# Optimization experiments

Measured on AMD Instinct MI355X. Metric: run time of the kernel, lower is better.

## Reference

```python
import jax, jax.numpy as jnp
import numpy as np

SR = 16000
N_FFT = 1024
HOP = 256
WIN = 1024
N_MELS = 80
EPS = 1e-8
DRY_W, RIR_W = 3.0, 1.0
TIME_W, FREQ_W, MEL_W = 1.0, 0.5, 0.3
CONSIST_W, RIR_REG_W = 0.2, 0.1


def _hann(n):
    # torch.hann_window(periodic=True)
    return (0.5 - 0.5 * jnp.cos(2.0 * jnp.pi * jnp.arange(n) / n)).astype(jnp.float32)


def _stft(x):
    """torchaudio.transforms.Spectrogram(power=None, normalized=True) equivalent.
    x: [..., T] -> complex [..., n_freqs, n_frames]"""
    shp = x.shape
    T = shp[-1]
    xf = x.reshape(-1, T)
    pad = N_FFT // 2
    xp = jnp.pad(xf, ((0, 0), (pad, pad)), mode='reflect')  # center=True
    n_frames = 1 + T // HOP
    idx = jnp.arange(n_frames)[:, None] * HOP + jnp.arange(N_FFT)[None, :]
    win = _hann(WIN)
    frames = xp[:, idx] * win[None, None, :]              # [N, frames, n_fft]
    spec = jnp.fft.rfft(frames, axis=-1)                  # [N, frames, freqs]
    spec = spec / jnp.sqrt(jnp.sum(win ** 2))             # normalized='window'
    return spec.reshape(shp[:-1] + (n_frames, N_FFT // 2 + 1)).swapaxes(-1, -2)


def _mel_fb():
    # torchaudio melscale_fbanks, htk scale, norm=None, f_min=0, f_max=sr/2
    n_freqs = N_FFT // 2 + 1
    all_freqs = np.linspace(0.0, SR / 2.0, n_freqs)
    hz2mel = lambda f: 2595.0 * np.log10(1.0 + f / 700.0)
    mel2hz = lambda m: 700.0 * (10.0 ** (m / 2595.0) - 1.0)
    m_pts = np.linspace(hz2mel(0.0), hz2mel(SR / 2.0), N_MELS + 2)
    f_pts = mel2hz(m_pts)
    f_diff = f_pts[1:] - f_pts[:-1]
    slopes = f_pts[None, :] - all_freqs[:, None]
    down = -slopes[:, :-2] / f_diff[:-1]
    up = slopes[:, 2:] / f_diff[1:]
    fb = np.maximum(0.0, np.minimum(down, up))
    return jnp.asarray(fb, jnp.float32)  # [n_freqs, n_mels]

_FB = _mel_fb()


def _l1(a, b):
    return jnp.mean(jnp.abs(a - b))


def _freq_loss(pred, target):
    ps, ts = _stft(pred), _stft(target)
    mag_loss = _l1(jnp.abs(ps), jnp.abs(ts))
    dphi = jnp.angle(ps) - jnp.angle(ts)
    # cosine sim of unit [cos, sin] vectors == cos(delta phase)
    phase_loss = 1.0 - jnp.mean(jnp.cos(dphi))
    return mag_loss + 0.1 * phase_loss


def _mel_loss(pred, target):
    pm = jnp.einsum('...ft,fm->...mt', jnp.abs(_stft(pred)) ** 2, _FB)
    tm = jnp.einsum('...ft,fm->...mt', jnp.abs(_stft(target)) ** 2, _FB)
    return _l1(jnp.log(pm + EPS), jnp.log(tm + EPS))


def _consistency_loss(pred_dry, pred_rir, mix):
    # full linear convolution along time, truncated to first T samples
    T = pred_dry.shape[-1]
    n = 2 * T
    D = jnp.fft.rfft(pred_dry, n=n, axis=-1)
    R = jnp.fft.rfft(pred_rir, n=n, axis=-1)
    rec = jnp.fft.irfft(D * R, n=n, axis=-1)[..., :T]
    return _l1(rec, mix[..., :T])


def _rir_reg_loss(pred_rir):
    T = pred_rir.shape[-1]
    sparsity = jnp.mean(jnp.abs(pred_rir))
    seg = T // 4
    decay = 0.0
    for i in range(3):
        e1 = jnp.mean(pred_rir[:, :, i * seg:(i + 1) * seg] ** 2)
        e2 = jnp.mean(pred_rir[:, :, (i + 1) * seg:(i + 2) * seg] ** 2)
        decay = decay + jax.nn.relu(e2 - 0.8 * e1)
    return sparsity + decay


def setup_inputs() -> dict:
    key = jax.random.key(0)
    ks = jax.random.split(key, 5)
    shape = (32, 2, 64000)
    names = ['pred_dry', 'pred_rir', 'target_dry', 'target_rir', 'mix']
    return {n: jax.random.normal(k, shape, dtype=jnp.float32) for n, k in zip(names, ks)}


def reference(pred_dry, pred_rir, target_dry, target_rir, mix):
    dry_time = _l1(pred_dry, target_dry)
    dry_freq = _freq_loss(pred_dry, target_dry)
    dry_mel = _mel_loss(pred_dry, target_dry)
    total_dry = TIME_W * dry_time + FREQ_W * dry_freq + MEL_W * dry_mel

    rir_time = _l1(pred_rir, target_rir)
    rir_reg = _rir_reg_loss(pred_rir)
    total_rir = rir_time + RIR_REG_W * rir_reg

    consist = _consistency_loss(pred_dry, pred_rir, mix)
    total = DRY_W * total_dry + RIR_W * total_rir + CONSIST_W * consist
    return total
```

## Files before the change

### kernel.cpp

```cpp
#include <hip/hip_runtime.h>
#include <math.h>

#define ROWS 64
#define TLEN 64000
#define NFR 251
#define NMELS 80
#define NFB 131072
#define PI2F 6.28318530717958647692f
#define PI_F 3.14159265358979323846f

__device__ double g_part[64][12];

__device__ constexpr int DR[16] = {0,4,8,12,1,5,9,13,2,6,10,14,3,7,11,15};
__device__ constexpr int RM[16] = {0,3,2,1,15,14,13,12,11,10,9,8,7,6,5,4};

__device__ inline int dr4(int i){ return ((i & 3) << 2) | (i >> 2); }
__device__ inline int SW(int k){ return k + (k >> 5); }

__device__ inline void atomAddD(double* p, double v){
  __hip_atomic_fetch_add(p, v, __ATOMIC_RELAXED, __HIP_MEMORY_SCOPE_AGENT);
}
__device__ inline int brev6(int x){ return (int)((unsigned)__brev((unsigned)x) >> 26); }
__device__ inline float2 cmul(float2 a, float2 b){
  return make_float2(a.x*b.x - a.y*b.y, a.x*b.y + a.y*b.x);
}
__device__ inline float wred(float v){
#pragma unroll
  for (int o = 32; o > 0; o >>= 1) v += __shfl_down(v, o, 64);
  return v;
}

__device__ inline void wave_fence(){
  asm volatile("s_waitcnt lgkmcnt(0)" ::: "memory");
  __builtin_amdgcn_sched_barrier(0);
}

template<int S, int N>
__device__ inline void fft64_lanes(float2* v, int l){
  float2 W[5];
#pragma unroll
  for (int si = 0; si < 5; ++si){
    int d = 32 >> si;
    float a = (float)S * PI_F * (float)(l & (d-1)) * (1.0f/(float)d);
    float sn, cs; __sincosf(a, &sn, &cs);
    W[si] = make_float2(cs, sn);
  }
#pragma unroll
  for (int si = 0; si < 6; ++si){
    int d = 32 >> si;
    bool hi = (l & d) != 0;
#pragma unroll
    for (int rr = 0; rr < N; ++rr){
      float2 x = v[rr];
      float tx = __shfl_xor(x.x, d, 64);
      float ty = __shfl_xor(x.y, d, 64);
      float sx = x.x + tx, sy = x.y + ty;
      float dx = tx - x.x, dy = ty - x.y;
      float rx, ry;
      if (si < 5){ rx = dx*W[si].x - dy*W[si].y; ry = dx*W[si].y + dy*W[si].x; }
      else       { rx = dx; ry = dy; }
      v[rr].x = hi ? rx : sx;
      v[rr].y = hi ? ry : sy;
    }
  }
}

template<int S>
__device__ inline void fft16_reg(float2* v){
  const float Sf = (float)S;
  const float C1 = 0.9238795325112867f, S1 = 0.3826834323650898f, C2 = 0.7071067811865476f;
  const float2 W1[4] = {{1.f,0.f},{C1,Sf*S1},{C2,Sf*C2},{S1,Sf*C1}};
  const float2 W2[4] = {{1.f,0.f},{C2,Sf*C2},{0.f,Sf},{-C2,Sf*C2}};
  const float2 W3[4] = {{1.f,0.f},{S1,Sf*C1},{-C2,Sf*C2},{-C1,-Sf*S1}};
#pragma unroll
  for (int j = 0; j < 4; ++j){
    float2 x0=v[j], x1=v[j+4], x2=v[j+8], x3=v[j+12];
    float2 t0={x0.x+x2.x, x0.y+x2.y}, t1={x0.x-x2.x, x0.y-x2.y};
    float2 t2={x1.x+x3.x, x1.y+x3.y}, t3={x1.x-x3.x, x1.y-x3.y};
    float2 y0={t0.x+t2.x, t0.y+t2.y};
    float2 y2={t0.x-t2.x, t0.y-t2.y};
    float2 y1={t1.x - Sf*t3.y, t1.y + Sf*t3.x};
    float2 y3={t1.x + Sf*t3.y, t1.y - Sf*t3.x};
    v[j]=y0; v[j+4]=cmul(y1,W1[j]); v[j+8]=cmul(y2,W2[j]); v[j+12]=cmul(y3,W3[j]);
  }
#pragma unroll
  for (int b = 0; b < 4; ++b){
    float2 x0=v[4*b], x1=v[4*b+1], x2=v[4*b+2], x3=v[4*b+3];
    float2 t0={x0.x+x2.x, x0.y+x2.y}, t1={x0.x-x2.x, x0.y-x2.y};
    float2 t2={x1.x+x3.x, x1.y+x3.y}, t3={x1.x-x3.x, x1.y-x3.y};
    v[4*b]   = make_float2(t0.x+t2.x, t0.y+t2.y);
    v[4*b+2] = make_float2(t0.x-t2.x, t0.y-t2.y);
    v[4*b+1] = make_float2(t1.x - Sf*t3.y, t1.y + Sf*t3.x);
    v[4*b+3] = make_float2(t1.x + Sf*t3.y, t1.y - Sf*t3.x);
  }
}

template<int S>
__device__ inline void fft128_wave(float2* v, int l){
  float2 a = {v[0].x+v[1].x, v[0].y+v[1].y};
  float2 b = {v[0].x-v[1].x, v[0].y-v[1].y};
  float ang = (float)S * PI_F * (float)l * (1.0f/64.0f);
  float sn, cs; __sincosf(ang, &sn, &cs);
  v[0] = a; v[1] = cmul(b, make_float2(cs, sn));
  fft64_lanes<S,2>(v, l);
}

template<int S>
__device__ inline void fft8p(float2* y){
  const float Sf = (float)S;
  const float C2 = 0.7071067811865476f;
  float2 t0={y[0].x+y[4].x, y[0].y+y[4].y};
  float2 t1={y[1].x+y[5].x, y[1].y+y[5].y};
  float2 t2={y[2].x+y[6].x, y[2].y+y[6].y};
  float2 t3={y[3].x+y[7].x, y[3].y+y[7].y};
  float2 u0={y[0].x-y[4].x, y[0].y-y[4].y};
  float2 u1={y[1].x-y[5].x, y[1].y-y[5].y};
  float2 u2={y[2].x-y[6].x, y[2].y-y[6].y};
  float2 u3={y[3].x-y[7].x, y[3].y-y[7].y};
  { float x=u1.x, yy=u1.y; u1.x = C2*(x - Sf*yy); u1.y = C2*(Sf*x + yy); }
  { float x=u2.x, yy=u2.y; u2.x = -Sf*yy;         u2.y = Sf*x; }
  { float x=u3.x, yy=u3.y; u3.x = -C2*(x + Sf*yy); u3.y = C2*(Sf*x - yy); }
  {
    float2 e0={t0.x+t2.x,t0.y+t2.y}, e1={t0.x-t2.x,t0.y-t2.y};
    float2 o0={t1.x+t3.x,t1.y+t3.y}, o1={t1.x-t3.x,t1.y-t3.y};
    y[0]=make_float2(e0.x+o0.x, e0.y+o0.y);
    y[4]=make_float2(e0.x-o0.x, e0.y-o0.y);
    y[2]=make_float2(e1.x - Sf*o1.y, e1.y + Sf*o1.x);
    y[6]=make_float2(e1.x + Sf*o1.y, e1.y - Sf*o1.x);
  }
  {
    float2 e0={u0.x+u2.x,u0.y+u2.y}, e1={u0.x-u2.x,u0.y-u2.y};
    float2 o0={u1.x+u3.x,u1.y+u3.y}, o1={u1.x-u3.x,u1.y-u3.y};
    y[1]=make_float2(e0.x+o0.x, e0.y+o0.y);
    y[5]=make_float2(e0.x-o0.x, e0.y-o0.y);
    y[3]=make_float2(e1.x - Sf*o1.y, e1.y + Sf*o1.x);
    y[7]=make_float2(e1.x + Sf*o1.y, e1.y - Sf*o1.x);
  }
}

template<int S>
__device__ inline void fft64_lds(float2* v, int l, float2* scr){
  int s = l >> 3, a = l & 7;
  int sw = (s & 1);
#pragma unroll
  for (int h = 0; h < 2; ++h){
    float2* vh = v + 8*h;
#pragma unroll
    for (int r = 0; r < 8; ++r) scr[r*64 + l] = vh[r];
    wave_fence();
    float2 y[8];
#pragma unroll
    for (int j = 0; j < 8; ++j)
      y[j] = scr[s*64 + a + 8*((j + s) & 7)];
    fft8p<S>(y);
    {
      float ang = (float)S * PI2F * (float)l * (1.0f/64.0f);
      float sn, cs; __sincosf(ang, &sn, &cs);
      float2 b1 = make_float2(cs, sn), cur = b1;
#pragma unroll
      for (int c = 1; c < 8; ++c){
        y[c] = cmul(y[c], cur);
        if (c < 7) cur = cmul(cur, b1);
      }
    }
    wave_fence();
#pragma unroll
    for (int c = 0; c < 8; ++c)
      scr[s*64 + a + 8*(c ^ sw)] = y[c];
    wave_fence();
    float2 z[8];
#pragma unroll
    for (int j = 0; j < 8; ++j)
      z[j] = scr[s*64 + ((j + s) & 7) + 8*(a ^ sw)];
    fft8p<S>(z);
    {
      float ang2 = (float)S * PI2F * (float)s * 0.125f;
      float sn2, cs2; __sincosf(ang2, &sn2, &cs2);
      float2 b2 = make_float2(cs2, sn2), cur = b2;
#pragma unroll
      for (int d = 1; d < 8; ++d){
        z[d] = cmul(z[d], cur);
        if (d < 7) cur = cmul(cur, b2);
      }
    }
    wave_fence();
#pragma unroll
    for (int d = 0; d < 8; ++d)
      scr[s*64 + a + 8*(d ^ sw)] = z[d];
    wave_fence();
#pragma unroll
    for (int r = 0; r < 8; ++r)
      vh[r] = scr[r*64 + (l ^ ((r & 1) << 3))];
    wave_fence();
  }
}

template<int S>
__device__ inline void fft1024_lds(float2* v, int l, float2* scr){
  fft16_reg<S>(v);
  float a = (float)S * PI2F * (float)l * (1.0f/1024.0f);
  float sn, cs; __sincosf(a, &sn, &cs);
  float2 T = make_float2(cs, sn);
  float2 cur = T;
#pragma unroll
  for (int k2 = 1; k2 < 16; ++k2){
    v[DR[k2]] = cmul(v[DR[k2]], cur);
    if (k2 < 15) cur = cmul(cur, T);
  }
  fft64_lds<S>(v, l, scr);
}

__device__ inline void r4p(float2* v, int i0, int i1, int i2, int i3){
  float2 x0=v[i0], x1=v[i1], x2=v[i2], x3=v[i3];
  float2 t0={x0.x+x2.x, x0.y+x2.y}, t1={x0.x-x2.x, x0.y-x2.y};
  float2 t2={x1.x+x3.x, x1.y+x3.y}, t3={x1.x-x3.x, x1.y-x3.y};
  v[i0] = make_float2(t0.x+t2.x, t0.y+t2.y);
  v[i2] = make_float2(t0.x-t2.x, t0.y-t2.y);
  v[i1] = make_float2(t1.x - t3.y, t1.y + t3.x);
  v[i3] = make_float2(t1.x + t3.y, t1.y - t3.x);
}

__device__ inline void ifft16_reg(float2* v){
#pragma unroll
  for (int b = 0; b < 4; ++b) r4p(v, 4*b, 4*b+1, 4*b+2, 4*b+3);
  const float C1 = 0.9238795325112867f, S1 = 0.3826834323650898f, C2 = 0.7071067811865476f;
  const float2 W1[4] = {{1.f,0.f},{C1,S1},{C2,C2},{S1,C1}};
  const float2 W2[4] = {{1.f,0.f},{C2,C2},{0.f,1.f},{-C2,C2}};
  const float2 W3[4] = {{1.f,0.f},{S1,C1},{-C2,C2},{-C1,-S1}};
#pragma unroll
  for (int j = 1; j < 4; ++j){
    v[j+4]  = cmul(v[j+4],  W1[j]);
    v[j+8]  = cmul(v[j+8],  W2[j]);
    v[j+12] = cmul(v[j+12], W3[j]);
  }
#pragma unroll
  for (int j = 0; j < 4; ++j) r4p(v, j, j+4, j+8, j+12);
}

__device__ inline void ifft1024_lds(float2* v, int l, float2* scr){
  fft64_lds<1>(v, l, scr);
  float a = PI2F * (float)l * (1.0f/1024.0f);
  float sn, cs; __sincosf(a, &sn, &cs);
  float2 T = make_float2(cs, sn);
  float2 cur = T;
#pragma unroll
  for (int k2 = 1; k2 < 16; ++k2){
    v[DR[k2]] = cmul(v[DR[k2]], cur);
    if (k2 < 15) cur = cmul(cur, T);
  }
  ifft16_reg(v);
}

template<int N>
__device__ inline void ifft64_lanes(float2* v, int l){
  float2 W[5];
#pragma unroll
  for (int si = 0; si < 5; ++si){
    int d = 32 >> si;
    float a = PI_F * (float)(l & (d-1)) * (1.0f/(float)d);
    float sn, cs; __sincosf(a, &sn, &cs);
    W[si] = make_float2(cs, sn);
  }
#pragma unroll
  for (int si = 5; si >= 0; --si){
    int d = 32 >> si;
    bool hi = (l & d) != 0;
#pragma unroll
    for (int rr = 0; rr < N; ++rr){
      float2 x = v[rr];
      float2 xp = x;
      if (si < 5 && hi) xp = cmul(x, W[si]);
      float tx = __shfl_xor(xp.x, d, 64);
      float ty = __shfl_xor(xp.y, d, 64);
      v[rr].x = hi ? (tx - xp.x) : (xp.x + tx);
      v[rr].y = hi ? (ty - xp.y) : (xp.y + ty);
    }
  }
}

__device__ inline void ifft128_wave(float2* v, int l){
  ifft64_lanes<2>(v, l);
  float ang = PI_F * (float)l * (1.0f/64.0f);
  float sn, cs; __sincosf(ang, &sn, &cs);
  v[1] = cmul(v[1], make_float2(cs, sn));
  float2 a = {v[0].x+v[1].x, v[0].y+v[1].y};
  float2 b = {v[0].x-v[1].x, v[0].y-v[1].y};
  v[0] = a; v[1] = b;
}

extern "C" __global__ void __launch_bounds__(256) k_init(){
  int t = blockIdx.x*256 + threadIdx.x;
  if (t < 768) ((double*)g_part)[t] = 0.0;
}

extern "C" __global__ void __launch_bounds__(256) k_time(
    const float* __restrict__ pd, const float* __restrict__ td,
    const float* __restrict__ pr, const float* __restrict__ tr){
  const int N4 = ROWS*TLEN/4;
  int stride = gridDim.x * 256;
  float sdt=0.f, srt=0.f, ssp=0.f, e0=0.f, e1=0.f, e2=0.f, e3=0.f;
  const float4* pd4 = (const float4*)pd;
  const float4* td4 = (const float4*)td;
  const float4* pr4 = (const float4*)pr;
  const float4* tr4 = (const float4*)tr;
  for (int i = blockIdx.x*256 + threadIdx.x; i < N4; i += stride){
    float4 a = pd4[i], b = td4[i], p = pr4[i], q = tr4[i];
    sdt += fabsf(a.x-b.x)+fabsf(a.y-b.y)+fabsf(a.z-b.z)+fabsf(a.w-b.w);
    srt += fabsf(p.x-q.x)+fabsf(p.y-q.y)+fabsf(p.z-q.z)+fabsf(p.w-q.w);
    ssp += fabsf(p.x)+fabsf(p.y)+fabsf(p.z)+fabsf(p.w);
    float p2 = p.x*p.x + p.y*p.y + p.z*p.z + p.w*p.w;
    int seg = (i % 16000) / 4000;
    if (seg == 0) e0 += p2; else if (seg == 1) e1 += p2;
    else if (seg == 2) e2 += p2; else e3 += p2;
  }
  sdt = wred(sdt); srt = wred(srt); ssp = wred(ssp);
  e0 = wred(e0); e1 = wred(e1); e2 = wred(e2); e3 = wred(e3);
  if ((threadIdx.x & 63) == 0){
    int bank = (blockIdx.x*4 + (threadIdx.x >> 6)) & 63;
    atomAddD(&g_part[bank][0], (double)sdt);
    atomAddD(&g_part[bank][1], (double)srt);
    atomAddD(&g_part[bank][2], (double)ssp);
    atomAddD(&g_part[bank][3], (double)e0);
    atomAddD(&g_part[bank][4], (double)e1);
    atomAddD(&g_part[bank][5], (double)e2);
    atomAddD(&g_part[bank][6], (double)e3);
  }
}

extern "C" __global__ void __launch_bounds__(64) k_stft(
    const float* __restrict__ pd, const float* __restrict__ td){
  __shared__ float2 scr[512];
  __shared__ float2 spec0[64];
  __shared__ float2 pt[530];
  int l = threadIdx.x;
  int frame = (blockIdx.x & 7) * (ROWS*NFR/8) + (blockIdx.x >> 3);
  int r = frame / NFR, fr = frame - r*NFR;
  const float* pdr = pd + (size_t)r*TLEN;
  const float* tdr = td + (size_t)r*TLEN;
  const float scale = 0.05103103630798288f;
  int base = fr*256 - 512;
  float2 v[16];
#pragma unroll
  for (int m = 0; m < 16; ++m){
    int j = l + 64*m;
    int g = base + j;
    g = (g < 0) ? -g : ((g >= TLEN) ? (2*TLEN - 2 - g) : g);
    float w = (0.5f - 0.5f*__cosf((PI2F/1024.0f)*(float)j)) * scale;
    v[m] = make_float2(pdr[g]*w, tdr[g]*w);
  }
  fft1024_lds<-1>(v, l, scr);
  spec0[l] = v[0];
  float magp = 0.f, cosp = 0.f;
#pragma unroll
  for (int rr = 1; rr < 16; ++rr){
    float2 z = v[rr];
    float2 zm;
    zm.x = __shfl_xor(v[RM[rr]].x, 63, 64);
    zm.y = __shfl_xor(v[RM[rr]].y, 63, 64);
    int k = DR[rr] + 16*l;
    float px = 0.5f*(z.x + zm.x), py = 0.5f*(z.y - zm.y);
    float tx = 0.5f*(z.y + zm.y), ty = -0.5f*(z.x - zm.x);
    float ppk = px*px + py*py, ttk = tx*tx + ty*ty;
    float rp = rsqrtf(fmaxf(ppk, 1e-30f)), rt = rsqrtf(fmaxf(ttk, 1e-30f));
    magp += 0.5f*fabsf(ppk*rp - ttk*rt);
    cosp += 0.5f*((px*tx + py*ty)*rp*rt);
    int kk = (k <= 512) ? k : 1024 - k;
    pt[SW(kk)] = make_float2(ppk, ttk);
  }
  if (l <= 32){
    float2 z  = spec0[l];
    float2 zm = spec0[(64 - l) & 63];
    float px = 0.5f*(z.x + zm.x), py = 0.5f*(z.y - zm.y);
    float tx = 0.5f*(z.y + zm.y), ty = -0.5f*(z.x - zm.x);
    float ppk = px*px + py*py, ttk = tx*tx + ty*ty;
    float rp = rsqrtf(fmaxf(ppk, 1e-30f)), rt = rsqrtf(fmaxf(ttk, 1e-30f));
    magp += fabsf(ppk*rp - ttk*rt);
    cosp += (px*tx + py*ty)*rp*rt;
    pt[SW(16*l)] = make_float2(ppk, ttk);
  }
  float melp = 0.f;
  const float C = (2595.0f * log10f(1.0f + 8000.0f/700.0f))
                  * (1.0f/81.0f) * (1.0f/2595.0f) * 2.302585093f;
  const float df = 15.625f;
  {
    int m = l;
    float f0 = 700.0f*(__expf(C*(float)(m  )) - 1.0f);
    float f1 = 700.0f*(__expf(C*(float)(m+1)) - 1.0f);
    float f2 = 700.0f*(__expf(C*(float)(m+2)) - 1.0f);
    float i1 = 1.0f/(f1 - f0), i2 = 1.0f/(f2 - f1);
    int lo = (int)ceilf(f0 * (1.0f/df));  if (lo < 0) lo = 0;
    int hi = (int)floorf(f2 * (1.0f/df)); if (hi > 512) hi = 512;
    float pm = 0.f, tm = 0.f;
#pragma unroll 2
    for (int k = lo; k <= hi; ++k){
      float frq = df*(float)k;
      float c = fmaxf(fminf((frq - f0)*i1, (f2 - frq)*i2), 0.f);
      float2 w = pt[SW(k)];
      pm += c*w.x; tm += c*w.y;
    }
    melp += fabsf(__logf(pm + 1e-8f) - __logf(tm + 1e-8f));
  }
  {
    int m = 64 + (l >> 2), q = l & 3;
    float f0 = 700.0f*(__expf(C*(float)(m  )) - 1.0f);
    float f1 = 700.0f*(__expf(C*(float)(m+1)) - 1.0f);
    float f2 = 700.0f*(__expf(C*(float)(m+2)) - 1.0f);
    float i1 = 1.0f/(f1 - f0), i2 = 1.0f/(f2 - f1);
    int lo = (int)ceilf(f0 * (1.0f/df));  if (lo < 0) lo = 0;
    int hi = (int)floorf(f2 * (1.0f/df)); if (hi > 512) hi = 512;
    int n = hi - lo + 1;
    int ch = (n + 3) >> 2;
    int k0 = lo + q*ch;
    int k1 = k0 + ch; if (k1 > hi + 1) k1 = hi + 1;
    float pm = 0.f, tm = 0.f;
#pragma unroll 2
    for (int k = k0; k < k1; ++k){
      float frq = df*(float)k;
      float c = fmaxf(fminf((frq - f0)*i1, (f2 - frq)*i2), 0.f);
      float2 w = pt[SW(k)];
      pm += c*w.x; tm += c*w.y;
    }
    pm += __shfl_xor(pm, 1, 64); pm += __shfl_xor(pm, 2, 64);
    tm += __shfl_xor(tm, 1, 64); tm += __shfl_xor(tm, 2, 64);
    if (q == 0)
      melp += fabsf(__logf(pm + 1e-8f) - __logf(tm + 1e-8f));
  }
  magp = wred(magp); cosp = wred(cosp); melp = wred(melp);
  if (l == 0){
    int bank = blockIdx.x & 63;
    atomAddD(&g_part[bank][7], (double)magp);
    atomAddD(&g_part[bank][8], (double)cosp);
    atomAddD(&g_part[bank][9], (double)melp);
  }
}

extern "C" __global__ void __launch_bounds__(512) k_fwd1(
    const float* __restrict__ pd, const float* __restrict__ pr,
    float2* __restrict__ buf, int row0){
  __shared__ float SM[10256];
  float* LA = SM;
  float* LB = SM + 5000;
  float2* LT = (float2*)SM;
  int wid = threadIdx.x >> 6, l = threadIdx.x & 63;
  int tid = threadIdx.x;
  float2* scr = (float2*)SM + (size_t)wid*512;
  int rl = blockIdx.y;
  int n1base = blockIdx.x * 8;
  int n1 = n1base + wid;
  const float* a = pd + (size_t)(row0+rl)*TLEN;
  const float* b = pr + (size_t)(row0+rl)*TLEN;
  for (int i = tid; i < 2000; i += 512){
    int n2 = i >> 2, wp = (i & 3)*2;
    float2 va = *(const float2*)&a[n1base + wp + 128*n2];
    float2 vb = *(const float2*)&b[n1base + wp + 128*n2];
    *(float2*)&LA[n2*10 + wp] = va;
    *(float2*)&LB[n2*10 + wp] = vb;
  }
  __syncthreads();
  float2 v[16];
#pragma unroll
  for (int m = 0; m < 16; ++m){
    int n2 = l + 64*m;
    if (n2 < 500) v[m] = make_float2(LA[n2*10 + wid], LB[n2*10 + wid]);
    else          v[m] = make_float2(0.f, 0.f);
  }
  __syncthreads();
  fft1024_lds<-1>(v, l, scr);
  const float tw = -(PI2F / (float)NFB);
#pragma unroll
  for (int rr = 0; rr < 16; ++rr){
    int K = DR[rr] + 16*l;
    float ang = tw * (float)(n1*K);
    float sn, cs; __sincosf(ang, &sn, &cs);
    v[rr] = cmul(v[rr], make_float2(cs, sn));
  }
  float2* rowp = buf + (size_t)rl*NFB;
  __syncthreads();
#pragma unroll
  for (int c = 0; c < 2; ++c){
#pragma unroll
    for (int rrl = 0; rrl < 8; ++rrl)
      LT[wid*513 + rrl*64 + l] = v[c*8 + rrl];
    __syncthreads();
#pragma unroll
    for (int it = 0; it < 4; ++it){
      int g = (tid + it*512)*2;
      int s = g >> 3, nw = g & 7;
      float2 x = LT[nw*513 + s], y = LT[(nw+1)*513 + s];
      *(float4*)&rowp[(size_t)(c*512 + s)*128 + n1base + nw] =
          make_float4(x.x, x.y, y.x, y.y);
    }
    __syncthreads();
  }
}

__device__ inline float2 pointmul(float2 z, float2 zm){
  float Dx = 0.5f*(z.x + zm.x), Dy = 0.5f*(z.y - zm.y);
  float Rx = 0.5f*(z.y + zm.y), Ry = -0.5f*(z.x - zm.x);
  return make_float2(Dx*Rx - Dy*Ry, Dx*Ry + Dy*Rx);
}

extern "C" __global__ void __launch_bounds__(256) k_mid(float2* __restrict__ buf){
  int wid = threadIdx.x >> 6, l = threadIdx.x & 63;
  int p = blockIdx.x*4 + wid;
  if (p > 512) return;
  int k2A = p, k2B = (1024 - p) & 1023;
  int sA = dr4(k2A & 15)*64 + (k2A >> 4);
  int sB = dr4(k2B & 15)*64 + (k2B >> 4);
  float2* base = buf + (size_t)blockIdx.y*NFB;
  float2* rA = base + (size_t)sA*128;
  float2* rB = base + (size_t)sB*128;
  bool pair = (sB != sA);
  float2 vA[2] = { rA[l], rA[l+64] };
  float2 vB[2];
  if (pair){ vB[0] = rB[l]; vB[1] = rB[l+64]; }
  fft128_wave<-1>(vA, l);
  if (pair) fft128_wave<-1>(vB, l);
  float2 cA[2];
  if (p == 0){
    int kb = brev6(l);
    int q0 = brev6((64 - kb) & 63);
    float2 zm0 = { __shfl(vA[0].x, q0, 64), __shfl(vA[0].y, q0, 64) };
    float2 zm1 = { __shfl_xor(vA[1].x, 63, 64), __shfl_xor(vA[1].y, 63, 64) };
    cA[0] = pointmul(vA[0], zm0);
    cA[1] = pointmul(vA[1], zm1);
  } else {
    const float2* src = pair ? vB : vA;
    float2 zm0 = { __shfl_xor(src[1].x, 63, 64), __shfl_xor(src[1].y, 63, 64) };
    float2 zm1 = { __shfl_xor(src[0].x, 63, 64), __shfl_xor(src[0].y, 63, 64) };
    cA[0] = pointmul(vA[0], zm0);
    cA[1] = pointmul(vA[1], zm1);
  }
  float2 cB[2];
  if (pair){
    cB[0] = make_float2( __shfl_xor(cA[1].x, 63, 64), -__shfl_xor(cA[1].y, 63, 64) );
    cB[1] = make_float2( __shfl_xor(cA[0].x, 63, 64), -__shfl_xor(cA[0].y, 63, 64) );
  }
  const float twi = PI2F / (float)NFB;
  ifft128_wave(cA, l);
#pragma unroll
  for (int rr = 0; rr < 2; ++rr){
    int n1 = l + 64*rr;
    float ang = twi * (float)(n1*k2A);
    float sn, cs; __sincosf(ang, &sn, &cs);
    rA[n1] = cmul(cA[rr], make_float2(cs, sn));
  }
  if (pair){
    ifft128_wave(cB, l);
#pragma unroll
    for (int rr = 0; rr < 2; ++rr){
      int n1 = l + 64*rr;
      float ang = twi * (float)(n1*k2B);
      float sn, cs; __sincosf(ang, &sn, &cs);
      rB[n1] = cmul(cB[rr], make_float2(cs, sn));
    }
  }
}

extern "C" __global__ void __launch_bounds__(512) k_inv2(
    const float* __restrict__ mix, float2* __restrict__ buf, int row0){
  __shared__ float SM[13208];
  float2* LT = (float2*)SM;
  float* LM = SM + 8208;
  int wid = threadIdx.x >> 6, l = threadIdx.x & 63;
  int tid = threadIdx.x;
  float2* scr = (float2*)SM + (size_t)wid*512;
  int rl = blockIdx.y;
  int n1base = blockIdx.x * 8;
  float2* rowp = buf + (size_t)rl*NFB;
  float2 v[16];
#pragma unroll
  for (int c = 0; c < 2; ++c){
#pragma unroll
    for (int it = 0; it < 4; ++it){
      int g = (tid + it*512)*2;
      int s = g >> 3, nw = g & 7;
      float4 q = *(const float4*)&rowp[(size_t)(c*512 + s)*128 + n1base + nw];
      LT[nw*513 + s]     = make_float2(q.x, q.y);
      LT[(nw+1)*513 + s] = make_float2(q.z, q.w);
    }
    __syncthreads();
#pragma unroll
    for (int rrl = 0; rrl < 8; ++rrl)
      v[c*8 + rrl] = LT[wid*513 + rrl*64 + l];
    __syncthreads();
  }
  const float* mr = mix + (size_t)(row0+rl)*TLEN;
  for (int i = tid; i < 2000; i += 512){
    int n2 = i >> 2, wp = (i & 3)*2;
    *(float2*)&LM[n2*10 + wp] = *(const float2*)&mr[n1base + wp + 128*n2];
  }
  ifft1024_lds(v, l, scr);
  __syncthreads();
  const float invn = 1.0f/(float)NFB;
  float acc = 0.f;
#pragma unroll
  for (int m = 0; m < 16; ++m){
    int n2 = l + 64*m;
    if (n2 < 500)
      acc += fabsf(v[m].x*invn - LM[n2*10 + wid]);
  }
  acc = wred(acc);
  if (l == 0){
    int bank = (blockIdx.x*8 + wid + blockIdx.y*16) & 63;
    atomAddD(&g_part[bank][10], (double)acc);
  }
}

extern "C" __global__ void __launch_bounds__(64) k_finalize(float* __restrict__ out){
  __shared__ double s[12];
  int t = threadIdx.x;
  if (t < 12){
    double v = 0.0;
    for (int b = 0; b < 64; ++b) v += g_part[b][t];
    s[t] = v;
  }
  __syncthreads();
  if (t == 0){
    double dt = s[0] / 4096000.0;
    double rt = s[1] / 4096000.0;
    double sp = s[2] / 4096000.0;
    double e0 = s[3] / 1024000.0, e1 = s[4] / 1024000.0;
    double e2 = s[5] / 1024000.0, e3 = s[6] / 1024000.0;
    double dec = fmax(e1 - 0.8*e0, 0.0) + fmax(e2 - 0.8*e1, 0.0) + fmax(e3 - 0.8*e2, 0.0);
    double c1 = 8240832.0;
    double freq = s[7]/c1 + 0.1*(1.0 - s[8]/c1);
    double mel  = s[9] / 1285120.0;
    double cons = s[10] / 4096000.0;
    double total = 3.0*(dt + 0.5*freq + 0.3*mel)
                 + (rt + 0.1*(sp + dec))
                 + 0.2*cons;
    out[0] = (float)total;
  }
}

extern "C" void kernel_launch(void* const* d_in, const int* in_sizes, int n_in,
                              void* d_out, int out_size, void* d_ws, size_t ws_size,
                              hipStream_t stream){
  const float* pd = (const float*)d_in[0];
  const float* pr = (const float*)d_in[1];
  const float* td = (const float*)d_in[2];
  const float* tr = (const float*)d_in[3];
  const float* mx = (const float*)d_in[4];
  float* out = (float*)d_out;
  float2* buf = (float2*)d_ws;

  size_t rowBytes = (size_t)NFB * sizeof(float2);
  int maxrows = (int)(ws_size / rowBytes);
  if (maxrows > ROWS) maxrows = ROWS;
  if (maxrows < 1) maxrows = 1;
  int nch = (ROWS + maxrows - 1) / maxrows;
  int chrows = (ROWS + nch - 1) / nch;

  hipLaunchKernelGGL(k_init, dim3(3), dim3(256), 0, stream);
  hipLaunchKernelGGL(k_time, dim3(2048), dim3(256), 0, stream, pd, td, pr, tr);
  hipLaunchKernelGGL(k_stft, dim3(ROWS*NFR), dim3(64), 0, stream, pd, td);
  for (int row0 = 0; row0 < ROWS; row0 += chrows){
    int nr = ROWS - row0; if (nr > chrows) nr = chrows;
    hipLaunchKernelGGL(k_fwd1, dim3(16, nr),  dim3(512), 0, stream, pd, pr, buf, row0);
    hipLaunchKernelGGL(k_mid,  dim3(129, nr), dim3(256), 0, stream, buf);
    hipLaunchKernelGGL(k_inv2, dim3(16, nr),  dim3(512), 0, stream, mx, buf, row0);
  }
  hipLaunchKernelGGL(k_finalize, dim3(1), dim3(64), 0, stream, out);
}
```

Measured before the change: 285.8 us.

## Pack two real inverse FFT columns into one complex IFFT in consistency loss

The inverse stage exploits the conjugate symmetry of real outputs. k_mid no longer runs a second 128-point IFFT for the paired column and instead writes the conjugate of the first. k_inv2 combines two adjacent columns as a + i*b into one complex sequence, runs half as many 1024-point IFFTs with 256 threads, and reads the real and imaginary parts as the two real time signals. It also drops a sched_barrier in wave_fence and picks power-of-two chunk row counts. This halves FFT work and LDS use in the inverse path, at the risk of subtle indexing or sign errors in the packing.

Measured after the change: 273.3 us. 1.05x faster.

```diff
diff --git a/kernel.cpp b/kernel.cpp
--- a/kernel.cpp
+++ b/kernel.cpp
@@ -32,7 +32,6 @@
 
 __device__ inline void wave_fence(){
   asm volatile("s_waitcnt lgkmcnt(0)" ::: "memory");
-  __builtin_amdgcn_sched_barrier(0);
 }
 
 template<int S, int N>
@@ -531,11 +530,6 @@
     cA[0] = pointmul(vA[0], zm0);
     cA[1] = pointmul(vA[1], zm1);
   }
-  float2 cB[2];
-  if (pair){
-    cB[0] = make_float2( __shfl_xor(cA[1].x, 63, 64), -__shfl_xor(cA[1].y, 63, 64) );
-    cB[1] = make_float2( __shfl_xor(cA[0].x, 63, 64), -__shfl_xor(cA[0].y, 63, 64) );
-  }
   const float twi = PI2F / (float)NFB;
   ifft128_wave(cA, l);
 #pragma unroll
@@ -543,25 +537,17 @@
     int n1 = l + 64*rr;
     float ang = twi * (float)(n1*k2A);
     float sn, cs; __sincosf(ang, &sn, &cs);
-    rA[n1] = cmul(cA[rr], make_float2(cs, sn));
-  }
-  if (pair){
-    ifft128_wave(cB, l);
-#pragma unroll
-    for (int rr = 0; rr < 2; ++rr){
-      int n1 = l + 64*rr;
-      float ang = twi * (float)(n1*k2B);
-      float sn, cs; __sincosf(ang, &sn, &cs);
-      rB[n1] = cmul(cB[rr], make_float2(cs, sn));
-    }
-  }
-}
-
-extern "C" __global__ void __launch_bounds__(512) k_inv2(
+    float2 val = cmul(cA[rr], make_float2(cs, sn));
+    rA[n1] = val;
+    if (pair) rB[n1] = make_float2(val.x, -val.y);
+  }
+}
+
+extern "C" __global__ void __launch_bounds__(256) k_inv2(
     const float* __restrict__ mix, float2* __restrict__ buf, int row0){
-  __shared__ float SM[13208];
+  __shared__ float SM[9104];
   float2* LT = (float2*)SM;
-  float* LM = SM + 8208;
+  float* LM = SM + 4104;
   int wid = threadIdx.x >> 6, l = threadIdx.x & 63;
   int tid = threadIdx.x;
   float2* scr = (float2*)SM + (size_t)wid*512;
@@ -572,12 +558,11 @@
 #pragma unroll
   for (int c = 0; c < 2; ++c){
 #pragma unroll
-    for (int it = 0; it < 4; ++it){
-      int g = (tid + it*512)*2;
+    for (int it = 0; it < 8; ++it){
+      int g = (tid + it*256)*2;
       int s = g >> 3, nw = g & 7;
       float4 q = *(const float4*)&rowp[(size_t)(c*512 + s)*128 + n1base + nw];
-      LT[nw*513 + s]     = make_float2(q.x, q.y);
-      LT[(nw+1)*513 + s] = make_float2(q.z, q.w);
+      LT[(nw >> 1)*513 + s] = make_float2(q.x - q.w, q.y + q.z);
     }
     __syncthreads();
 #pragma unroll
@@ -586,7 +571,7 @@
     __syncthreads();
   }
   const float* mr = mix + (size_t)(row0+rl)*TLEN;
-  for (int i = tid; i < 2000; i += 512){
+  for (int i = tid; i < 2000; i += 256){
     int n2 = i >> 2, wp = (i & 3)*2;
     *(float2*)&LM[n2*10 + wp] = *(const float2*)&mr[n1base + wp + 128*n2];
   }
@@ -597,12 +582,14 @@
 #pragma unroll
   for (int m = 0; m < 16; ++m){
     int n2 = l + 64*m;
-    if (n2 < 500)
-      acc += fabsf(v[m].x*invn - LM[n2*10 + wid]);
+    if (n2 < 500){
+      float2 mm = *(const float2*)&LM[n2*10 + 2*wid];
+      acc += fabsf(v[m].x*invn - mm.x) + fabsf(v[m].y*invn - mm.y);
+    }
   }
   acc = wred(acc);
   if (l == 0){
-    int bank = (blockIdx.x*8 + wid + blockIdx.y*16) & 63;
+    int bank = (blockIdx.x*4 + wid + blockIdx.y*16) & 63;
     atomAddD(&g_part[bank][10], (double)acc);
   }
 }
@@ -649,8 +636,9 @@
   int maxrows = (int)(ws_size / rowBytes);
   if (maxrows > ROWS) maxrows = ROWS;
   if (maxrows < 1) maxrows = 1;
-  int nch = (ROWS + maxrows - 1) / maxrows;
-  int chrows = (ROWS + nch - 1) / nch;
+  int chrows = 1;
+  const int cand[7] = {64, 32, 16, 8, 4, 2, 1};
+  for (int i = 0; i < 7; ++i) if (cand[i] <= maxrows){ chrows = cand[i]; break; }
 
   hipLaunchKernelGGL(k_init, dim3(3), dim3(256), 0, stream);
   hipLaunchKernelGGL(k_time, dim3(2048), dim3(256), 0, stream, pd, td, pr, tr);
@@ -659,7 +647,7 @@
     int nr = ROWS - row0; if (nr > chrows) nr = chrows;
     hipLaunchKernelGGL(k_fwd1, dim3(16, nr),  dim3(512), 0, stream, pd, pr, buf, row0);
     hipLaunchKernelGGL(k_mid,  dim3(129, nr), dim3(256), 0, stream, buf);
-    hipLaunchKernelGGL(k_inv2, dim3(16, nr),  dim3(512), 0, stream, mx, buf, row0);
+    hipLaunchKernelGGL(k_inv2, dim3(16, nr),  dim3(256), 0, stream, mx, buf, row0);
   }
   hipLaunchKernelGGL(k_finalize, dim3(1), dim3(64), 0, stream, out);
 }
```
